# Kernel optimization log

Hardware: AMD Instinct MI355X
Metric: run time of the kernel (lower is better)

Reference implementation:

```python
import jax, jax.numpy as jnp
import numpy as np

B, N, C_FEAT = 2, 1024, 64
S, K, K_FP = 512, 32, 3
D_MODEL, N_HEAD = 128, 4
EPS_BN = 1e-5


def square_distance(src, dst):
    # src [B,N,3], dst [B,M,3] -> [B,N,M], same expansion as torch version
    d = -2.0 * jnp.einsum('bnc,bmc->bnm', src, dst)
    d = d + jnp.sum(src ** 2, -1)[:, :, None]
    d = d + jnp.sum(dst ** 2, -1)[:, None, :]
    return d


def gather_points(points, idx):
    # points [B,N,C], idx [B,...] int -> [B,...,C]  (index_points)
    return jax.vmap(lambda p, i: p[i])(points, idx)


def fps(xyz, n_samples):
    # furthest point sampling, deterministic start at index 0
    Bs, Np, _ = xyz.shape
    def step(carry, _):
        dist, far = carry
        centroid = jax.vmap(lambda p, i: p[i])(xyz, far)  # [B,3]
        d = jnp.sum((xyz - centroid[:, None, :]) ** 2, -1)
        dist = jnp.minimum(dist, d)
        new_far = jnp.argmax(dist, -1).astype(jnp.int32)
        return (dist, new_far), far
    init = (jnp.full((Bs, Np), 1e10, xyz.dtype), jnp.zeros((Bs,), jnp.int32))
    _, idxs = jax.lax.scan(step, init, None, length=n_samples)
    return idxs.T  # [B,S]


def knn(nsample, xyz, new_xyz):
    d = square_distance(new_xyz, xyz)
    _, idx = jax.lax.top_k(-d, nsample)
    return idx  # [B, n_query, nsample]


def setup_inputs() -> dict:
    key = jax.random.key(0)
    ks = jax.random.split(key, 12)
    Din = 2 * C_FEAT + 3  # 131 = 3 + 2*channels (PreExtraction in_channels)
    def lin(k, fan_in, shape):
        return (jax.random.normal(k, shape, jnp.float32) / np.sqrt(fan_in)).astype(jnp.float32)
    z = lambda n: jnp.zeros((n,), jnp.float32)
    return {
        'xyz': jax.random.normal(ks[0], (B, N, 3), jnp.float32),
        'feats': jax.random.normal(ks[1], (B, N, C_FEAT), jnp.float32),
        'affine_alpha': jnp.ones((1, 1, 1, C_FEAT + 3), jnp.float32),
        'affine_beta': jnp.zeros((1, 1, 1, C_FEAT + 3), jnp.float32),
        'W_t': lin(ks[2], Din, (Din, D_MODEL)), 'b_t': z(D_MODEL),
        'bn_g': jnp.ones((D_MODEL,), jnp.float32), 'bn_b': z(D_MODEL),
        'Wq': lin(ks[3], D_MODEL, (D_MODEL, D_MODEL)), 'bq': z(D_MODEL),
        'Wk': lin(ks[4], D_MODEL, (D_MODEL, D_MODEL)), 'bk': z(D_MODEL),
        'Wv': lin(ks[5], D_MODEL, (D_MODEL, D_MODEL)), 'bv': z(D_MODEL),
        'Wo': lin(ks[6], D_MODEL, (D_MODEL, D_MODEL)), 'bo': z(D_MODEL),
        'Wp1': lin(ks[7], 3, (3, D_MODEL)), 'bp1': z(D_MODEL),
        'Wp2': lin(ks[8], D_MODEL, (D_MODEL, N_HEAD)), 'bp2': z(N_HEAD),
    }


def reference(xyz, feats, affine_alpha, affine_beta, W_t, b_t, bn_g, bn_b,
              Wq, bq, Wk, bk, Wv, bv, Wo, bo, Wp1, bp1, Wp2, bp2):
    # ---- LocalGrouper (FPS + KNN + gather + center-normalize + affine) ----
    fps_idx = fps(xyz, S)                       # [B,S]
    new_xyz = gather_points(xyz, fps_idx)       # [B,S,3]
    anchor_feats = gather_points(feats, fps_idx)  # [B,S,C]
    idx = knn(K, xyz, new_xyz)                  # [B,S,K]
    grouped_xyz = gather_points(xyz, idx)       # [B,S,K,3]
    grouped_pts = gather_points(feats, idx)     # [B,S,K,C]
    grouped = jnp.concatenate([grouped_pts, grouped_xyz], -1)  # [B,S,K,C+3]
    mean = jnp.mean(grouped, axis=2, keepdims=True)
    std = jnp.std((grouped - mean).reshape(B, -1), axis=-1, ddof=1)[:, None, None, None]
    grouped = (grouped - mean) / (std + 1e-5)
    grouped = affine_alpha * grouped + affine_beta
    anchor_rep = jnp.broadcast_to(anchor_feats[:, :, None, :], (B, S, K, C_FEAT))
    new_points = jnp.concatenate([grouped, anchor_rep], -1)  # [B,S,K,2C+3]
    # ---- PreExtraction transfer (1x1 conv + BN(eval) + ReLU) + max over K ----
    y = jnp.einsum('bskd,do->bsko', new_points, W_t) + b_t
    y = y * (bn_g / jnp.sqrt(1.0 + EPS_BN)) + bn_b  # BN with running stats (0,1)
    y = jax.nn.relu(y)
    v_k = jnp.max(y, axis=2)                    # [B,S,D_MODEL]
    # ---- PointNetFeaturePropagation (KNN-3 inverse-distance interp) ----
    idx_fp = knn(K_FP, new_xyz, xyz)            # [B,N,3]
    sqrd = square_distance(xyz, new_xyz)        # [B,N,S]
    d_near = jnp.clip(jnp.take_along_axis(sqrd, idx_fp, axis=2), 1e-10, None)
    w = 1.0 / d_near
    w = w / jnp.sum(w, -1, keepdims=True)
    grouped_v = gather_points(v_k, idx_fp)      # [B,N,3,D]
    v_q = jnp.einsum('bnk,bnkc->bnc', w, grouped_v)  # [B,N,D]
    # ---- PointTransformerCrossAttention ----
    Dh = D_MODEL // N_HEAD
    qh = (v_q @ Wq + bq).reshape(B, N, N_HEAD, Dh)
    kh = (v_k @ Wk + bk).reshape(B, S, N_HEAD, Dh)
    vh = (v_k @ Wv + bv).reshape(B, S, N_HEAD, Dh)
    rel = xyz[:, :, None, :] - new_xyz[:, None, :, :]         # [B,N,S,3]
    rpe = jax.nn.relu(rel @ Wp1 + bp1) @ Wp2 + bp2            # [B,N,S,H]
    energy = jnp.einsum('bihd,bjhd->bhij', qh, kh) / jnp.sqrt(jnp.float32(Dh))
    attn = jax.nn.softmax(energy + rpe.transpose(0, 3, 1, 2), axis=-1)
    out = jnp.einsum('bhij,bjhd->bihd', attn, vh).reshape(B, N, D_MODEL)
    return out @ Wo + bo
```

## Files before the change

kernel.cpp:

```cpp
#include <hip/hip_runtime.h>
#include <math.h>

namespace {

constexpr int B  = 2;
constexpr int N  = 1024;
constexpr int CF = 64;
constexpr int S  = 512;
constexpr int K  = 32;
constexpr int DM = 128;
constexpr int NH = 4;
constexpr int DH = 32;
constexpr int GC = 67;
constexpr int DIN = 131;
constexpr int DPAD = 132;
constexpr int EPAD = 516;

typedef float f2 __attribute__((ext_vector_type(2)));

__device__ inline float max3f(float a, float b, float c) { return fmaxf(fmaxf(a, b), c); }
__device__ inline unsigned min3u(unsigned a, unsigned b, unsigned c) { return min(min(a, b), c); }

template <int CTRL>
__device__ inline float dpp_mov_f(float v) {
  return __int_as_float(__builtin_amdgcn_update_dpp(0, __float_as_int(v), CTRL, 0xF, 0xF, true));
}
template <int CTRL>
__device__ inline unsigned dpp_mov_self_u(unsigned v) {
  return (unsigned)__builtin_amdgcn_update_dpp((int)v, (int)v, CTRL, 0xF, 0xF, false);
}

__global__ void __launch_bounds__(64, 1)
fps_kernel(const float* __restrict__ xyz, int* __restrict__ fps_idx,
           float* __restrict__ new_xyz) {
  const int b = blockIdx.x;
  const int lane = threadIdx.x;
  __shared__ __align__(16) float4 pts4[N];
  __shared__ int farhist[S];
  for (int p = lane; p < N; p += 64) {
    pts4[p] = make_float4(xyz[b*N*3 + p*3+0], xyz[b*N*3 + p*3+1], xyz[b*N*3 + p*3+2], 0.0f);
  }
  __syncthreads();
  f2 X[8], Y[8], Z[8];
  float dist[16];
  #pragma unroll
  for (int j = 0; j < 8; ++j) {
    const float4 a = pts4[(2*j)*64 + lane];
    const float4 c = pts4[(2*j+1)*64 + lane];
    X[j] = f2{a.x, c.x}; Y[j] = f2{a.y, c.y}; Z[j] = f2{a.z, c.z};
  }
  #pragma unroll
  for (int k = 0; k < 16; ++k) dist[k] = 1e10f;
  int far = 0;
  for (int s = 0; s < S; ++s) {
    if (lane == 0) farhist[s] = far;
    const float4 c = pts4[far];
    const f2 cx = f2{c.x, c.x}, cy = f2{c.y, c.y}, cz = f2{c.z, c.z};
    #pragma unroll
    for (int j = 0; j < 8; ++j) {
      const f2 dx = X[j] - cx, dy = Y[j] - cy, dz = Z[j] - cz;
      const f2 q = dx*dx + dy*dy + dz*dz;
      dist[2*j]   = fminf(dist[2*j],   q.x);
      dist[2*j+1] = fminf(dist[2*j+1], q.y);
    }
    const float l0 = max3f(dist[0],  dist[1],  dist[2]);
    const float l1 = max3f(dist[3],  dist[4],  dist[5]);
    const float l2 = max3f(dist[6],  dist[7],  dist[8]);
    const float l3 = max3f(dist[9],  dist[10], dist[11]);
    const float l4 = max3f(dist[12], dist[13], dist[14]);
    float mv = fmaxf(max3f(l0, l1, l2), max3f(l3, l4, dist[15]));
    mv = fmaxf(mv, dpp_mov_f<0x111>(mv));
    mv = fmaxf(mv, dpp_mov_f<0x112>(mv));
    mv = fmaxf(mv, dpp_mov_f<0x114>(mv));
    mv = fmaxf(mv, dpp_mov_f<0x118>(mv));
    mv = fmaxf(mv, dpp_mov_f<0x142>(mv));
    mv = fmaxf(mv, dpp_mov_f<0x143>(mv));
    const float maxv = __int_as_float(__builtin_amdgcn_readlane(__float_as_int(mv), 63));
    unsigned cnd[16];
    #pragma unroll
    for (int k = 0; k < 16; ++k) {
      cnd[k] = (dist[k] == maxv) ? (unsigned)(k*64 + lane) : 0xFFFFFFFFu;
    }
    const unsigned u0 = min3u(cnd[0],  cnd[1],  cnd[2]);
    const unsigned u1 = min3u(cnd[3],  cnd[4],  cnd[5]);
    const unsigned u2 = min3u(cnd[6],  cnd[7],  cnd[8]);
    const unsigned u3 = min3u(cnd[9],  cnd[10], cnd[11]);
    const unsigned u4 = min3u(cnd[12], cnd[13], cnd[14]);
    unsigned cand = min(min3u(u0, u1, u2), min3u(u3, u4, cnd[15]));
    cand = min(cand, dpp_mov_self_u<0x111>(cand));
    cand = min(cand, dpp_mov_self_u<0x112>(cand));
    cand = min(cand, dpp_mov_self_u<0x114>(cand));
    cand = min(cand, dpp_mov_self_u<0x118>(cand));
    cand = min(cand, dpp_mov_self_u<0x142>(cand));
    cand = min(cand, dpp_mov_self_u<0x143>(cand));
    far = __builtin_amdgcn_readlane((int)cand, 63);
  }
  __syncthreads();
  for (int s = lane; s < S; s += 64) {
    const int f = farhist[s];
    const float4 c = pts4[f];
    fps_idx[b*S+s] = f;
    new_xyz[(b*S+s)*3+0] = c.x;
    new_xyz[(b*S+s)*3+1] = c.y;
    new_xyz[(b*S+s)*3+2] = c.z;
  }
}

__global__ void knn_kernel(const float* __restrict__ xyz, const float* __restrict__ feats,
                           const float* __restrict__ new_xyz, int* __restrict__ knn_idx,
                           float* __restrict__ mean_out, float2* __restrict__ partials) {
  const int b = blockIdx.y;
  const int tid = threadIdx.x;
  const int wave = tid >> 6, lane = tid & 63;
  const int s = blockIdx.x * 4 + wave;
  __shared__ float pts[N*3];
  __shared__ int sidx_s[4][K];
  for (int i = tid; i < N*3; i += 256) pts[i] = xyz[b*N*3 + i];
  __syncthreads();
  const float qx = new_xyz[(b*S+s)*3+0], qy = new_xyz[(b*S+s)*3+1], qz = new_xyz[(b*S+s)*3+2];
  const float qn = qx*qx + qy*qy + qz*qz;
  float d[16];
  #pragma unroll
  for (int j = 0; j < 16; ++j) {
    const int p = j*64 + lane;
    const float px = pts[p*3+0], py = pts[p*3+1], pz = pts[p*3+2];
    const float dot = qx*px + qy*py + qz*pz;
    const float pn  = px*px + py*py + pz*pz;
    d[j] = (-2.0f*dot + qn) + pn;
  }
  unsigned mask = 0xFFFFu;
  for (int k = 0; k < K; ++k) {
    float bv = INFINITY; int bj = 0;
    #pragma unroll
    for (int j = 0; j < 16; ++j) {
      if (((mask >> j) & 1u) && d[j] < bv) { bv = d[j]; bj = j; }
    }
    int bp = bj*64 + lane;
    #pragma unroll
    for (int m = 1; m < 64; m <<= 1) {
      const float ov = __shfl_xor(bv, m);
      const int   op = __shfl_xor(bp, m);
      if (ov < bv || (ov == bv && op < bp)) { bv = ov; bp = op; }
    }
    if (lane == 0) { knn_idx[(b*S+s)*K + k] = bp; sidx_s[wave][k] = bp; }
    if ((bp & 63) == lane) mask &= ~(1u << (bp >> 6));
  }
  const int bs = b*S + s;
  float ls = 0.0f, lsq = 0.0f;
  float v[K];
  {
    const int c = lane;
    float sum = 0.0f;
    #pragma unroll
    for (int k = 0; k < K; ++k) {
      const int p = sidx_s[wave][k];
      const float g = feats[(b*N+p)*CF + c];
      v[k] = g; sum += g;
    }
    const float mean = sum * (1.0f/K);
    mean_out[bs*GC + c] = mean;
    #pragma unroll
    for (int k = 0; k < K; ++k) {
      const float cc = v[k] - mean;
      ls += cc; lsq += cc*cc;
    }
  }
  if (lane < 3) {
    const int c = CF + lane;
    float sum = 0.0f;
    #pragma unroll
    for (int k = 0; k < K; ++k) {
      const int p = sidx_s[wave][k];
      const float g = xyz[(b*N+p)*3 + lane];
      v[k] = g; sum += g;
    }
    const float mean = sum * (1.0f/K);
    mean_out[bs*GC + c] = mean;
    #pragma unroll
    for (int k = 0; k < K; ++k) {
      const float cc = v[k] - mean;
      ls += cc; lsq += cc*cc;
    }
  }
  #pragma unroll
  for (int m = 1; m < 64; m <<= 1) { ls += __shfl_xor(ls, m); lsq += __shfl_xor(lsq, m); }
  if (lane == 0) partials[bs] = make_float2(ls, lsq);
}

__global__ void stats_kernel(const float2* __restrict__ partials, float* __restrict__ invstd) {
  const int b = blockIdx.x;
  const int lane = threadIdx.x;
  double su = 0.0, sq = 0.0;
  for (int i = lane; i < S; i += 64) {
    const float2 p = partials[b*S+i];
    su += (double)p.x; sq += (double)p.y;
  }
  #pragma unroll
  for (int m = 1; m < 64; m <<= 1) { su += __shfl_xor(su, m); sq += __shfl_xor(sq, m); }
  if (lane == 0) {
    const double nn = (double)S * K * GC;
    const double var = (sq - su*su/nn) / (nn - 1.0);
    invstd[b] = 1.0f / ((float)sqrt(var) + 1e-5f);
  }
}

__global__ void transfer_kernel(const float* __restrict__ feats, const float* __restrict__ xyz,
                                const int* __restrict__ knn_idx, const int* __restrict__ fps_idx,
                                const float* __restrict__ mean_in, const float* __restrict__ invstd,
                                const float* __restrict__ alpha, const float* __restrict__ beta,
                                const float* __restrict__ W_t, const float* __restrict__ b_t,
                                const float* __restrict__ bn_g, const float* __restrict__ bn_b,
                                const float* __restrict__ Wk, const float* __restrict__ bk,
                                const float* __restrict__ Wv, const float* __restrict__ bv,
                                float* __restrict__ v_k, float* __restrict__ kpb,
                                float* __restrict__ vpb) {
  const int bs = blockIdx.x;
  const int b = bs / S;
  const int t = threadIdx.x;
  __shared__ __align__(16) float np_s[K][DPAD];
  __shared__ float vrow[DM];
  __shared__ int sidx[K];
  __shared__ int sanchor;
  if (t < K) sidx[t] = knn_idx[bs*K + t];
  if (t == 0) sanchor = fps_idx[bs];
  __syncthreads();
  const float sinv = invstd[b];
  for (int k = 0; k < K; ++k) {
    const int p = sidx[k];
    for (int c = t; c < DPAD; c += 128) {
      float val = 0.0f;
      if (c < GC) {
        const float g = (c < CF) ? feats[(b*N+p)*CF + c] : xyz[(b*N+p)*3 + (c-CF)];
        val = (g - mean_in[bs*GC + c]) * sinv * alpha[c] + beta[c];
      } else if (c < DIN) {
        val = feats[(b*N+sanchor)*CF + (c - GC)];
      }
      np_s[k][c] = val;
    }
  }
  __syncthreads();
  float acc[K];
  const float bt = b_t[t];
  #pragma unroll
  for (int k = 0; k < K; ++k) acc[k] = bt;
  for (int d4 = 0; d4 < DPAD/4; ++d4) {
    const int d = d4*4;
    const float w0 = W_t[(d+0)*DM + t];
    const float w1 = W_t[(d+1)*DM + t];
    const float w2 = W_t[(d+2)*DM + t];
    const float w3 = (d+3 < DIN) ? W_t[(d+3)*DM + t] : 0.0f;
    #pragma unroll
    for (int k = 0; k < K; ++k) {
      const float4 f = *reinterpret_cast<const float4*>(&np_s[k][d]);
      acc[k] = acc[k] + f.x*w0 + f.y*w1 + f.z*w2 + f.w*w3;
    }
  }
  const float scale = bn_g[t] / sqrtf(1.0f + 1e-5f);
  const float shift = bn_b[t];
  float mx = -INFINITY;
  #pragma unroll
  for (int k = 0; k < K; ++k) {
    const float y = fmaxf(acc[k]*scale + shift, 0.0f);
    mx = fmaxf(mx, y);
  }
  v_k[bs*DM + t] = mx;
  vrow[t] = mx;
  __syncthreads();
  float acck = bk[t], accv = bv[t];
  for (int d = 0; d < DM; ++d) {
    const float f = vrow[d];
    acck += f * Wk[d*DM + t];
    accv += f * Wv[d*DM + t];
  }
  kpb[bs*DM + t] = acck;
  vpb[bs*DM + t] = accv;
}

__global__ void interp_kernel(const float* __restrict__ xyz, const float* __restrict__ new_xyz,
                              const float* __restrict__ v_k, const float* __restrict__ Wq,
                              const float* __restrict__ bq, float* __restrict__ qbuf) {
  const int b = blockIdx.y;
  const int tid = threadIdx.x;
  const int wave = tid >> 6, lane = tid & 63;
  const int n = blockIdx.x*4 + wave;
  __shared__ float pts[S*3];
  __shared__ float vqs[4][DM];
  for (int i = tid; i < S*3; i += 256) pts[i] = new_xyz[b*S*3 + i];
  __syncthreads();
  const float qx = xyz[(b*N+n)*3+0], qy = xyz[(b*N+n)*3+1], qz = xyz[(b*N+n)*3+2];
  const float qn = qx*qx + qy*qy + qz*qz;
  float d[8];
  #pragma unroll
  for (int j = 0; j < 8; ++j) {
    const int p = j*64 + lane;
    const float px = pts[p*3+0], py = pts[p*3+1], pz = pts[p*3+2];
    const float dot = qx*px + qy*py + qz*pz;
    const float pn  = px*px + py*py + pz*pz;
    d[j] = (-2.0f*dot + qn) + pn;
  }
  unsigned mask = 0xFFu;
  float sd[3]; int sp[3];
  #pragma unroll
  for (int k = 0; k < 3; ++k) {
    float bv = INFINITY; int bj = 0;
    #pragma unroll
    for (int j = 0; j < 8; ++j) {
      if (((mask >> j) & 1u) && d[j] < bv) { bv = d[j]; bj = j; }
    }
    int bp = bj*64 + lane;
    #pragma unroll
    for (int m = 1; m < 64; m <<= 1) {
      const float ov = __shfl_xor(bv, m);
      const int   op = __shfl_xor(bp, m);
      if (ov < bv || (ov == bv && op < bp)) { bv = ov; bp = op; }
    }
    sd[k] = bv; sp[k] = bp;
    if ((bp & 63) == lane) mask &= ~(1u << (bp >> 6));
  }
  float w0 = 1.0f / fmaxf(sd[0], 1e-10f);
  float w1 = 1.0f / fmaxf(sd[1], 1e-10f);
  float w2 = 1.0f / fmaxf(sd[2], 1e-10f);
  const float wsum = w0 + w1 + w2;
  w0 /= wsum; w1 /= wsum; w2 /= wsum;
  const float* vk0 = v_k + (b*S + sp[0])*DM;
  const float* vk1 = v_k + (b*S + sp[1])*DM;
  const float* vk2 = v_k + (b*S + sp[2])*DM;
  #pragma unroll
  for (int c = lane; c < DM; c += 64) {
    vqs[wave][c] = w0*vk0[c] + w1*vk1[c] + w2*vk2[c];
  }
  __syncthreads();
  const float* row = vqs[wave];
  #pragma unroll
  for (int half = 0; half < 2; ++half) {
    const int c = lane + half*64;
    float acc = bq[c];
    for (int d = 0; d < DM; ++d) acc += row[d] * Wq[d*DM + c];
    qbuf[(b*N+n)*DM + c] = acc;
  }
}

__global__ void attn_kernel(const float* __restrict__ xyz, const float* __restrict__ new_xyz,
                            const float* __restrict__ qb, const float* __restrict__ kp,
                            const float* __restrict__ vp, const float* __restrict__ Wp1,
                            const float* __restrict__ bp1, const float* __restrict__ Wp2,
                            const float* __restrict__ bp2, const float* __restrict__ Wo,
                            const float* __restrict__ bo, float* __restrict__ out) {
  const int bn = blockIdx.x;
  const int b = bn / N;
  const int t = threadIdx.x;
  __shared__ __align__(16) float e[NH][EPAD];
  __shared__ float qn_s[DM];
  __shared__ __align__(16) float oa4[4][DM];
  __shared__ float ssum[NH];
  if (t < DM) qn_s[t] = qb[bn*DM + t];
  __syncthreads();
  const float qx = xyz[bn*3+0], qy = xyz[bn*3+1], qz = xyz[bn*3+2];
  const float rs = 0.17677669529663687f;
  {
    const int j = t;
    const float px = new_xyz[(b*S+j)*3+0], py = new_xyz[(b*S+j)*3+1], pz = new_xyz[(b*S+j)*3+2];
    const float rx = qx-px, ry = qy-py, rz = qz-pz;
    float r0 = bp2[0], r1 = bp2[1], r2 = bp2[2], r3 = bp2[3];
    for (int m = 0; m < DM; ++m) {
      float hm = rx*Wp1[m] + ry*Wp1[DM+m] + rz*Wp1[2*DM+m] + bp1[m];
      hm = fmaxf(hm, 0.0f);
      r0 += hm*Wp2[m*NH+0]; r1 += hm*Wp2[m*NH+1];
      r2 += hm*Wp2[m*NH+2]; r3 += hm*Wp2[m*NH+3];
    }
    const float rpe[NH] = {r0, r1, r2, r3};
    #pragma unroll
    for (int h = 0; h < NH; ++h) {
      const float4* kr4 = reinterpret_cast<const float4*>(kp + (b*S+j)*DM + h*DH);
      const float* qr = qn_s + h*DH;
      float acc = 0.0f;
      #pragma unroll
      for (int dd = 0; dd < 8; ++dd) {
        const float4 kv = kr4[dd];
        acc += qr[dd*4+0]*kv.x + qr[dd*4+1]*kv.y + qr[dd*4+2]*kv.z + qr[dd*4+3]*kv.w;
      }
      e[h][j] = acc*rs + rpe[h];
    }
  }
  __syncthreads();
  if (t < 128) {
    const int h = t >> 5, g = t & 31;
    float mx = -INFINITY;
    for (int j = g; j < S; j += 32) mx = fmaxf(mx, e[h][j]);
    #pragma unroll
    for (int m = 16; m >= 1; m >>= 1) mx = fmaxf(mx, __shfl_xor(mx, m));
    float sum = 0.0f;
    for (int j = g; j < S; j += 32) { const float ex = expf(e[h][j]-mx); e[h][j] = ex; sum += ex; }
    #pragma unroll
    for (int m = 16; m >= 1; m >>= 1) sum += __shfl_xor(sum, m);
    if (g == 0) ssum[h] = sum;
  }
  __syncthreads();
  {
    const int grp = t >> 7;
    const int tt = t & 127;
    const int h = tt >> 5;
    float acc = 0.0f;
    const int j0 = grp*128;
    for (int j = j0; j < j0 + 128; j += 4) {
      const float4 ev = *reinterpret_cast<const float4*>(&e[h][j]);
      acc += ev.x * vp[(b*S+j+0)*DM + tt];
      acc += ev.y * vp[(b*S+j+1)*DM + tt];
      acc += ev.z * vp[(b*S+j+2)*DM + tt];
      acc += ev.w * vp[(b*S+j+3)*DM + tt];
    }
    oa4[grp][tt] = acc;
  }
  __syncthreads();
  if (t < 128) {
    const int h = t >> 5;
    const float total = ((oa4[0][t] + oa4[1][t]) + oa4[2][t]) + oa4[3][t];
    oa4[0][t] = total / ssum[h];
  }
  __syncthreads();
  if (t < 128) {
    float facc = bo[t];
    for (int d = 0; d < DM; ++d) facc += oa4[0][d] * Wo[d*DM + t];
    out[bn*DM + t] = facc;
  }
}

}

extern "C" void kernel_launch(void* const* d_in, const int* in_sizes, int n_in,
                              void* d_out, int out_size, void* d_ws, size_t ws_size,
                              hipStream_t stream) {
  const float* xyz   = (const float*)d_in[0];
  const float* feats = (const float*)d_in[1];
  const float* alpha = (const float*)d_in[2];
  const float* beta  = (const float*)d_in[3];
  const float* W_t   = (const float*)d_in[4];
  const float* b_t   = (const float*)d_in[5];
  const float* bn_g  = (const float*)d_in[6];
  const float* bn_b  = (const float*)d_in[7];
  const float* Wq = (const float*)d_in[8];  const float* bq = (const float*)d_in[9];
  const float* Wk = (const float*)d_in[10]; const float* bk = (const float*)d_in[11];
  const float* Wv = (const float*)d_in[12]; const float* bv = (const float*)d_in[13];
  const float* Wo = (const float*)d_in[14]; const float* bo = (const float*)d_in[15];
  const float* Wp1= (const float*)d_in[16]; const float* bp1= (const float*)d_in[17];
  const float* Wp2= (const float*)d_in[18]; const float* bp2= (const float*)d_in[19];

  char* w = (char*)d_ws;
  int*    fps_i = (int*)   (w + 0);
  float*  nxyz  = (float*) (w + 4096);
  int*    knn_i = (int*)   (w + 16384);
  float*  meanb = (float*) (w + 147456);
  float2* part  = (float2*)(w + 421888);
  float*  invs  = (float*) (w + 430080);
  float*  vk    = (float*) (w + 430336);
  float*  qbuf  = (float*) (w + 2003200);
  float*  kpb   = (float*) (w + 3051776);
  float*  vpb   = (float*) (w + 3576064);
  float*  outf  = (float*)d_out;

  fps_kernel<<<B, 64, 0, stream>>>(xyz, fps_i, nxyz);
  knn_kernel<<<dim3(S/4, B), 256, 0, stream>>>(xyz, feats, nxyz, knn_i, meanb, part);
  stats_kernel<<<B, 64, 0, stream>>>(part, invs);
  transfer_kernel<<<B*S, 128, 0, stream>>>(feats, xyz, knn_i, fps_i, meanb, invs,
                                           alpha, beta, W_t, b_t, bn_g, bn_b,
                                           Wk, bk, Wv, bv, vk, kpb, vpb);
  interp_kernel<<<dim3(N/4, B), 256, 0, stream>>>(xyz, nxyz, vk, Wq, bq, qbuf);
  attn_kernel<<<B*N, 512, 0, stream>>>(xyz, nxyz, qbuf, kpb, vpb, Wp1, bp1, Wp2, bp2, Wo, bo, outf);
}
```

Baseline: 423.6 us.

## Process four queries per attention block to reuse key/value loads and weights

The attention kernel now handles four query points per block instead of one, so each thread's key row loads, RPE weight loads and value loads are shared across four queries. The softmax, PV product and output projection are redistributed so each 128-thread group owns one query, which removes the cross-group partial-sum reduction and one barrier. This cuts grid size by four and raises per-thread register and LDS use, which may lower occupancy. Each thread also now walks all 512 keys serially in the PV loop.

```diff
diff --git a/kernel.cpp b/kernel.cpp
--- a/kernel.cpp
+++ b/kernel.cpp
@@ -15,6 +15,7 @@
 constexpr int DIN = 131;
 constexpr int DPAD = 132;
 constexpr int EPAD = 516;
+constexpr int QB = 4;
 
 typedef float f2 __attribute__((ext_vector_type(2)));
 
@@ -346,82 +347,96 @@
                             const float* __restrict__ bp1, const float* __restrict__ Wp2,
                             const float* __restrict__ bp2, const float* __restrict__ Wo,
                             const float* __restrict__ bo, float* __restrict__ out) {
-  const int bn = blockIdx.x;
-  const int b = bn / N;
+  const int bn0 = blockIdx.x * QB;
+  const int b = bn0 / N;
   const int t = threadIdx.x;
-  __shared__ __align__(16) float e[NH][EPAD];
-  __shared__ float qn_s[DM];
-  __shared__ __align__(16) float oa4[4][DM];
-  __shared__ float ssum[NH];
-  if (t < DM) qn_s[t] = qb[bn*DM + t];
-  __syncthreads();
-  const float qx = xyz[bn*3+0], qy = xyz[bn*3+1], qz = xyz[bn*3+2];
+  __shared__ __align__(16) float e[QB][NH][EPAD];
+  __shared__ __align__(16) float qn_s[QB][DM];
+  __shared__ float oa[QB][DM];
+  __shared__ float ssum[QB][NH];
+  qn_s[t >> 7][t & 127] = qb[(bn0 + (t >> 7))*DM + (t & 127)];
+  __syncthreads();
+  float qxs[QB], qys[QB], qzs[QB];
+  #pragma unroll
+  for (int qq = 0; qq < QB; ++qq) {
+    qxs[qq] = xyz[(bn0+qq)*3+0];
+    qys[qq] = xyz[(bn0+qq)*3+1];
+    qzs[qq] = xyz[(bn0+qq)*3+2];
+  }
   const float rs = 0.17677669529663687f;
   {
     const int j = t;
     const float px = new_xyz[(b*S+j)*3+0], py = new_xyz[(b*S+j)*3+1], pz = new_xyz[(b*S+j)*3+2];
-    const float rx = qx-px, ry = qy-py, rz = qz-pz;
-    float r0 = bp2[0], r1 = bp2[1], r2 = bp2[2], r3 = bp2[3];
+    float rx[QB], ry[QB], rz[QB];
+    float r0[QB], r1[QB], r2[QB], r3[QB];
+    #pragma unroll
+    for (int qq = 0; qq < QB; ++qq) {
+      rx[qq] = qxs[qq]-px; ry[qq] = qys[qq]-py; rz[qq] = qzs[qq]-pz;
+      r0[qq] = bp2[0]; r1[qq] = bp2[1]; r2[qq] = bp2[2]; r3[qq] = bp2[3];
+    }
     for (int m = 0; m < DM; ++m) {
-      float hm = rx*Wp1[m] + ry*Wp1[DM+m] + rz*Wp1[2*DM+m] + bp1[m];
-      hm = fmaxf(hm, 0.0f);
-      r0 += hm*Wp2[m*NH+0]; r1 += hm*Wp2[m*NH+1];
-      r2 += hm*Wp2[m*NH+2]; r3 += hm*Wp2[m*NH+3];
-    }
-    const float rpe[NH] = {r0, r1, r2, r3};
+      const float w1 = Wp1[m], w2 = Wp1[DM+m], w3 = Wp1[2*DM+m], bb = bp1[m];
+      const float p0 = Wp2[m*NH+0], p1 = Wp2[m*NH+1], p2 = Wp2[m*NH+2], p3 = Wp2[m*NH+3];
+      #pragma unroll
+      for (int qq = 0; qq < QB; ++qq) {
+        float hm = rx[qq]*w1 + ry[qq]*w2 + rz[qq]*w3 + bb;
+        hm = fmaxf(hm, 0.0f);
+        r0[qq] += hm*p0; r1[qq] += hm*p1; r2[qq] += hm*p2; r3[qq] += hm*p3;
+      }
+    }
     #pragma unroll
     for (int h = 0; h < NH; ++h) {
       const float4* kr4 = reinterpret_cast<const float4*>(kp + (b*S+j)*DM + h*DH);
-      const float* qr = qn_s + h*DH;
-      float acc = 0.0f;
+      float acc[QB];
+      #pragma unroll
+      for (int qq = 0; qq < QB; ++qq) acc[qq] = 0.0f;
       #pragma unroll
       for (int dd = 0; dd < 8; ++dd) {
         const float4 kv = kr4[dd];
-        acc += qr[dd*4+0]*kv.x + qr[dd*4+1]*kv.y + qr[dd*4+2]*kv.z + qr[dd*4+3]*kv.w;
+        #pragma unroll
+        for (int qq = 0; qq < QB; ++qq) {
+          const float* qr = &qn_s[qq][h*DH + dd*4];
+          acc[qq] += qr[0]*kv.x + qr[1]*kv.y + qr[2]*kv.z + qr[3]*kv.w;
+        }
       }
-      e[h][j] = acc*rs + rpe[h];
-    }
-  }
-  __syncthreads();
-  if (t < 128) {
-    const int h = t >> 5, g = t & 31;
+      e[0][h][j] = acc[0]*rs + ((h==0)?r0[0]:(h==1)?r1[0]:(h==2)?r2[0]:r3[0]);
+      e[1][h][j] = acc[1]*rs + ((h==0)?r0[1]:(h==1)?r1[1]:(h==2)?r2[1]:r3[1]);
+      e[2][h][j] = acc[2]*rs + ((h==0)?r0[2]:(h==1)?r1[2]:(h==2)?r2[2]:r3[2]);
+      e[3][h][j] = acc[3]*rs + ((h==0)?r0[3]:(h==1)?r1[3]:(h==2)?r2[3]:r3[3]);
+    }
+  }
+  __syncthreads();
+  const int qq = t >> 7;
+  const int tt = t & 127;
+  const int h = tt >> 5, g = tt & 31;
+  {
     float mx = -INFINITY;
-    for (int j = g; j < S; j += 32) mx = fmaxf(mx, e[h][j]);
+    for (int j = g; j < S; j += 32) mx = fmaxf(mx, e[qq][h][j]);
     #pragma unroll
     for (int m = 16; m >= 1; m >>= 1) mx = fmaxf(mx, __shfl_xor(mx, m));
     float sum = 0.0f;
-    for (int j = g; j < S; j += 32) { const float ex = expf(e[h][j]-mx); e[h][j] = ex; sum += ex; }
+    for (int j = g; j < S; j += 32) { const float ex = expf(e[qq][h][j]-mx); e[qq][h][j] = ex; sum += ex; }
     #pragma unroll
     for (int m = 16; m >= 1; m >>= 1) sum += __shfl_xor(sum, m);
-    if (g == 0) ssum[h] = sum;
+    if (g == 0) ssum[qq][h] = sum;
   }
   __syncthreads();
   {
-    const int grp = t >> 7;
-    const int tt = t & 127;
-    const int h = tt >> 5;
     float acc = 0.0f;
-    const int j0 = grp*128;
-    for (int j = j0; j < j0 + 128; j += 4) {
-      const float4 ev = *reinterpret_cast<const float4*>(&e[h][j]);
+    for (int j = 0; j < S; j += 4) {
+      const float4 ev = *reinterpret_cast<const float4*>(&e[qq][h][j]);
       acc += ev.x * vp[(b*S+j+0)*DM + tt];
       acc += ev.y * vp[(b*S+j+1)*DM + tt];
       acc += ev.z * vp[(b*S+j+2)*DM + tt];
       acc += ev.w * vp[(b*S+j+3)*DM + tt];
     }
-    oa4[grp][tt] = acc;
-  }
-  __syncthreads();
-  if (t < 128) {
-    const int h = t >> 5;
-    const float total = ((oa4[0][t] + oa4[1][t]) + oa4[2][t]) + oa4[3][t];
-    oa4[0][t] = total / ssum[h];
-  }
-  __syncthreads();
-  if (t < 128) {
-    float facc = bo[t];
-    for (int d = 0; d < DM; ++d) facc += oa4[0][d] * Wo[d*DM + t];
-    out[bn*DM + t] = facc;
+    oa[qq][tt] = acc / ssum[qq][h];
+  }
+  __syncthreads();
+  {
+    float facc = bo[tt];
+    for (int d = 0; d < DM; ++d) facc += oa[qq][d] * Wo[d*DM + tt];
+    out[(bn0+qq)*DM + tt] = facc;
   }
 }
 
@@ -465,5 +480,5 @@
                                            alpha, beta, W_t, b_t, bn_g, bn_b,
                                            Wk, bk, Wv, bv, vk, kpb, vpb);
   interp_kernel<<<dim3(N/4, B), 256, 0, stream>>>(xyz, nxyz, vk, Wq, bq, qbuf);
-  attn_kernel<<<B*N, 512, 0, stream>>>(xyz, nxyz, qbuf, kpb, vpb, Wp1, bp1, Wp2, bp2, Wo, bo, outf);
-}
+  attn_kernel<<<(B*N)/QB, 512, 0, stream>>>(xyz, nxyz, qbuf, kpb, vpb, Wp1, bp1, Wp2, bp2, Wo, bo, outf);
+}
```

Measured after the change: 381.6 us, median of 2. -9.9%, faster.
